# Performance work log

Hardware: AMD Instinct MI355X
Metric: run time of the kernel (lower is better)

Reference implementation:

```python
import jax, jax.numpy as jnp
import numpy as np

B, NF, EMB = 2048, 32, 64
FEAT_MAP_DIM = [128, 128, 128]  # split_half=True, activation=None


def setup_inputs() -> dict:
    key = jax.random.key(0)
    ks = jax.random.split(key, 7)
    inp = jax.random.normal(ks[0], (B, NF, EMB), dtype=jnp.float32)
    # conv1d_i: in_channels = H_{i-1} * NF, out_channels = FEAT_MAP_DIM[i]
    # H_0 = NF = 32; H_1 = H_2 = 128 // 2 = 64 (split_half)
    in_chs = [NF * NF, (FEAT_MAP_DIM[0] // 2) * NF, (FEAT_MAP_DIM[1] // 2) * NF]
    params = {}
    for i, (ic, oc) in enumerate(zip(in_chs, FEAT_MAP_DIM)):
        bound = 1.0 / np.sqrt(ic)  # torch Conv1d default init range
        params[f"W{i}"] = jax.random.uniform(ks[1 + 2 * i], (oc, ic), jnp.float32, -bound, bound)
        params[f"b{i}"] = jax.random.uniform(ks[2 + 2 * i], (oc,), jnp.float32, -bound, bound)
    return {"inp": inp, **params}


def reference(inp, W0, b0, W1, b1, W2, b2):
    # CIN: h_k[b,o,e] = sum_{j,z} W_k[o, j*NF+z] * h_{k-1}[b,j,e] * inp[b,z,e] + b_k[o]
    # The torch code materializes the outer product then applies a 1x1 conv;
    # the fused triple einsum below computes identical math.
    nf = inp.shape[1]
    Ws, bs = [W0, W1, W2], [b0, b1, b2]
    h = inp
    outs = []
    n_layers = len(Ws)
    for i, (W, b) in enumerate(zip(Ws, bs)):
        O, Hj = W.shape[0], h.shape[1]
        Wr = W.reshape(O, Hj, nf)  # channel index c = j*nf + z
        nxt = jnp.einsum('bjk,bzk,ojz->bok', h, inp, Wr) + b[None, :, None]
        if i != n_layers - 1:  # split_half
            h, o = nxt[:, : O // 2], nxt[:, O // 2 :]
        else:
            o = nxt
        outs.append(o)
    out = jnp.concatenate(outs, axis=1)  # (B, 64+64+128, EMB)
    return jnp.sum(out, axis=2)  # (B, 256)
```

## Files before the change

kernel.cpp:

```cpp
#include <hip/hip_runtime.h>


typedef _Float16 f16;
typedef _Float16 f16x4 __attribute__((ext_vector_type(4)));
typedef _Float16 f16x8 __attribute__((ext_vector_type(8)));
typedef float f32x4 __attribute__((ext_vector_type(4)));
typedef float f32x16 __attribute__((ext_vector_type(16)));

#define HSTR 72
#define PBS  5120

__device__ __forceinline__ f32x16 zero16() {
    f32x16 v;
#pragma unroll
    for (int i = 0; i < 16; ++i) v[i] = 0.0f;
    return v;
}

__global__ void __launch_bounds__(256)
prep_frag(const float* __restrict__ W0, const float* __restrict__ W1,
          const float* __restrict__ W2, f16* __restrict__ dst)
{
    int g = (blockIdx.x * 256 + threadIdx.x) * 8;
    const float* src; int base, KK, rbase;
    if (g < 65536)       { src = W0; base = 0;      KK = 64;  rbase = 0;  }
    else if (g < 131072) { src = W0; base = 65536;  KK = 64;  rbase = 64; }
    else if (g < 262144) { src = W1; base = 131072; KK = 128; rbase = 0;  }
    else if (g < 393216) { src = W1; base = 262144; KK = 128; rbase = 64; }
    else                 { src = W2; base = 393216; KK = 128; rbase = 0;  }
    int local = g - base;
    int frag  = local >> 9;
    int lane  = (local >> 3) & 63;
    int kk    = frag % KK;
    int mc    = frag / KK;
    int row   = rbase + mc * 32 + (lane & 31);
    int col   = kk * 16 + (lane >> 5) * 8;
    int IC    = KK * 16;
    const float* s = src + (size_t)row * IC + col;
    f16x8 o;
#pragma unroll
    for (int i = 0; i < 8; ++i) o[i] = (f16)s[i];
    *(f16x8*)(dst + g) = o;
}

__device__ __forceinline__ void p_chunk(const f16* __restrict__ hrows,
                                        const f16x8 (&pB)[4],
                                        f16* __restrict__ pdst, int t, int q)
{
    f32x16 acc = zero16();
#pragma unroll
    for (int s = 0; s < 4; ++s) {
        f16x8 a = *(const f16x8*)(hrows + t * HSTR + s * 16 + q * 8);
        acc = __builtin_amdgcn_mfma_f32_32x32x16_f16(a, pB[s], acc, 0, 0, 0);
    }
#pragma unroll
    for (int r = 0; r < 16; ++r) {
        int row = (r & 3) + 8 * (r >> 2) + 4 * q;
        pdst[row * 32 + t] = (f16)acc[r];
    }
}

template <int HJ>
__device__ __forceinline__ void h_gemm2(const f16* __restrict__ Hf,
                                        const f16* __restrict__ h0,
                                        const f16* __restrict__ h1,
                                        int lane8, int khOff,
                                        const f16x8 (&ip)[2][2],
                                        f32x16 (&acc)[2])
{
    acc[0] = zero16(); acc[1] = zero16();
    const f16* Wp = Hf + lane8;
    f16x8 wb[2][4];
    f16   sc[2][4];
#pragma unroll
    for (int ph = 0; ph < 2; ++ph)
#pragma unroll
        for (int jr = 0; jr < 2; ++jr) {
            int j = ph * 2 + jr;
            wb[ph][jr*2+0] = *(const f16x8*)(Wp + (j * 2 + 0) * 512);
            wb[ph][jr*2+1] = *(const f16x8*)(Wp + (j * 2 + 1) * 512);
            sc[ph][jr*2+0] = h0[j * HSTR + khOff];
            sc[ph][jr*2+1] = h1[j * HSTR + khOff];
        }
    for (int jj = 0; jj < HJ; jj += 4) {
#pragma unroll
        for (int ph = 0; ph < 2; ++ph) {
#pragma unroll
            for (int jr = 0; jr < 2; ++jr) {
                f16x8 w0 = wb[ph][jr*2+0], w1 = wb[ph][jr*2+1];
                f16 s0 = sc[ph][jr*2+0], s1 = sc[ph][jr*2+1];
                acc[0] = __builtin_amdgcn_mfma_f32_32x32x16_f16(w0, ip[0][0] * s0, acc[0], 0, 0, 0);
                acc[1] = __builtin_amdgcn_mfma_f32_32x32x16_f16(w0, ip[1][0] * s1, acc[1], 0, 0, 0);
                acc[0] = __builtin_amdgcn_mfma_f32_32x32x16_f16(w1, ip[0][1] * s0, acc[0], 0, 0, 0);
                acc[1] = __builtin_amdgcn_mfma_f32_32x32x16_f16(w1, ip[1][1] * s1, acc[1], 0, 0, 0);
            }
            int jn = jj + 4 + ph * 2;
            if (jn > HJ - 2) jn = HJ - 2;
#pragma unroll
            for (int jr = 0; jr < 2; ++jr) {
                int j = jn + jr;
                wb[ph][jr*2+0] = *(const f16x8*)(Wp + (j * 2 + 0) * 512);
                wb[ph][jr*2+1] = *(const f16x8*)(Wp + (j * 2 + 1) * 512);
                sc[ph][jr*2+0] = h0[j * HSTR + khOff];
                sc[ph][jr*2+1] = h1[j * HSTR + khOff];
            }
        }
    }
}

__device__ __forceinline__ void load_bias(const float* __restrict__ bl,
                                          float (&bve)[16], int g, int q)
{
#pragma unroll
    for (int r = 0; r < 16; ++r)
        bve[r] = bl[g * 32 + (r & 3) + 8 * (r >> 2) + 4 * q];
}

__device__ __forceinline__ void epi2(const f32x16 (&acc)[2], f16* __restrict__ hL,
                                     const float (&bve)[16], int g, int khOff,
                                     int t, int q)
{
#pragma unroll
    for (int r = 0; r < 16; ++r) {
        int row = g * 32 + (r & 3) + 8 * (r >> 2) + 4 * q;
        hL[row * HSTR + khOff]              = (f16)(acc[0][r] + bve[r]);
        hL[64 * HSTR + row * HSTR + khOff]  = (f16)(acc[1][r] + bve[r]);
    }
}

__global__ void __launch_bounds__(256, 4)
cin_h(const float* __restrict__ inp, const f16* __restrict__ Wf,
      f16* __restrict__ pW,
      const float* __restrict__ b0v, const float* __restrict__ b1v)
{
    __shared__ __attribute__((aligned(16))) f16 hL[2 * 64 * HSTR];

    const int tid   = threadIdx.x;
    const int w     = tid >> 6;
    const int lane  = tid & 63;
    const int t     = lane & 31;
    const int q     = lane >> 5;
    const int lane8 = lane * 8;
    const int kh    = w & 1;
    const int g     = w >> 1;
    const int khOff = kh * 32 + t;
    const int b0i   = blockIdx.x * 2;

#pragma unroll
    for (int it = 0; it < 4; ++it) {
        int idx = it * 1024 + tid * 4;
        int b = idx >> 11, rem = idx & 2047;
        int z = rem >> 6, k = rem & 63;
        f32x4 v = *(const f32x4*)(inp + (size_t)(b0i + b) * 2048 + rem);
        f16x4 h4;
        h4[0] = (f16)v[0]; h4[1] = (f16)v[1]; h4[2] = (f16)v[2]; h4[3] = (f16)v[3];
        *(f16x4*)(hL + b * 64 * HSTR + z * HSTR + k) = h4;
    }
    __syncthreads();

    f16x8 ip[2][2];
#pragma unroll
    for (int b = 0; b < 2; ++b)
#pragma unroll
        for (int kq = 0; kq < 2; ++kq) {
            f16x8 v;
            const f16* src = hL + b * 64 * HSTR;
#pragma unroll
            for (int i = 0; i < 8; ++i)
                v[i] = src[(kq * 16 + q * 8 + i) * HSTR + khOff];
            ip[b][kq] = v;
        }
    f16x8 pB[4];
#pragma unroll
    for (int s = 0; s < 4; ++s)
        pB[s] = *(const f16x8*)(hL + kh * 64 * HSTR + t * HSTR + s * 16 + q * 8);

    f16* pMy = pW + (size_t)(b0i + kh) * PBS;
    const f16* H0 = Wf;
    const f16* H1 = Wf + 131072;
    f32x16 acc[2];
    float bve[16];

    if (g == 0)
        p_chunk(hL + kh * 64 * HSTR, pB, pMy, t, q);
    h_gemm2<32>(H0 + g * 64 * 512, hL, hL + 64 * HSTR, lane8, khOff, ip, acc);
    load_bias(b0v, bve, g, q);
    __syncthreads();
    epi2(acc, hL, bve, g, khOff, t, q);
    __syncthreads();

    p_chunk(hL + kh * 64 * HSTR + g * 32 * HSTR, pB, pMy + 1024 + g * 1024, t, q);
    h_gemm2<64>(H1 + g * 128 * 512, hL, hL + 64 * HSTR, lane8, khOff, ip, acc);
    load_bias(b1v, bve, g, q);
    __syncthreads();
    epi2(acc, hL, bve, g, khOff, t, q);
    __syncthreads();

    p_chunk(hL + kh * 64 * HSTR + g * 32 * HSTR, pB, pMy + 3072 + g * 1024, t, q);
}

template <int S>
__device__ __forceinline__ void o_tile(const f16* __restrict__ Of,
                                       const f16* __restrict__ pBase,
                                       const float* __restrict__ biasp,
                                       float* __restrict__ out,
                                       float* __restrict__ rP,
                                       int bg, int colbase, int tid)
{
    const int w = tid >> 6, lane = tid & 63, t = lane & 31, q = lane >> 5;
    const int lane8 = lane * 8;
    const int mi = w & 1, ki = w >> 1;
    const f16* Ap = Of + (size_t)(mi * 2 * S + ki * S) * 512 + lane8;
    const f16* Bp = pBase + (size_t)(bg * 32 + t) * PBS + ki * S * 16 + q * 8;

    f32x16 acc = zero16();
    f16x8 af[4], bf[4];
#pragma unroll
    for (int i = 0; i < 4; ++i) {
        af[i] = *(const f16x8*)(Ap + i * 512);
        bf[i] = *(const f16x8*)(Bp + i * 16);
    }
#pragma unroll 4
    for (int s = 0; s < S; ++s) {
        int idx = s & 3;
        f16x8 a = af[idx], b = bf[idx];
        int sn = s + 4 < S ? s + 4 : S - 1;
        af[idx] = *(const f16x8*)(Ap + sn * 512);
        bf[idx] = *(const f16x8*)(Bp + sn * 16);
        acc = __builtin_amdgcn_mfma_f32_32x32x16_f16(a, b, acc, 0, 0, 0);
    }
#pragma unroll
    for (int r = 0; r < 16; ++r) {
        int m = mi * 32 + (r & 3) + 8 * (r >> 2) + 4 * q;
        rP[(ki * 32 + t) * 64 + m] = acc[r];
    }
    __syncthreads();
#pragma unroll
    for (int it = 0; it < 2; ++it) {
        int idx4 = (it * 256 + tid) * 4;
        int n = idx4 >> 6, o = idx4 & 63;
        f32x4 v0 = *(const f32x4*)(rP + n * 64 + o);
        f32x4 v1 = *(const f32x4*)(rP + (32 + n) * 64 + o);
        f32x4 bb = *(const f32x4*)(biasp + o);
        f32x4 ov;
        ov[0] = v0[0] + v1[0] + 64.0f * bb[0];
        ov[1] = v0[1] + v1[1] + 64.0f * bb[1];
        ov[2] = v0[2] + v1[2] + 64.0f * bb[2];
        ov[3] = v0[3] + v1[3] + 64.0f * bb[3];
        *(f32x4*)(out + (size_t)(bg * 32 + n) * 256 + colbase + o) = ov;
    }
}

__global__ void __launch_bounds__(256, 2)
cin_out(const f16* __restrict__ Wf, const f16* __restrict__ pW,
        const float* __restrict__ b0v, const float* __restrict__ b1v,
        const float* __restrict__ b2v, float* __restrict__ out)
{
    __shared__ __attribute__((aligned(16))) float rP[2 * 32 * 64];
    const int tid = threadIdx.x;
    const int r  = blockIdx.x & 3;
    const int bg = blockIdx.x >> 2;
    if (r == 0)
        o_tile<32>(Wf + 65536,  pW,        b0v + 64, out, rP, bg, 0,   tid);
    else if (r == 1)
        o_tile<64>(Wf + 262144, pW + 1024, b1v + 64, out, rP, bg, 64,  tid);
    else if (r == 2)
        o_tile<64>(Wf + 393216, pW + 3072, b2v,      out, rP, bg, 128, tid);
    else
        o_tile<64>(Wf + 524288, pW + 3072, b2v + 64, out, rP, bg, 192, tid);
}

extern "C" void kernel_launch(void* const* d_in, const int* in_sizes, int n_in,
                              void* d_out, int out_size, void* d_ws, size_t ws_size,
                              hipStream_t stream)
{
    const float* inp = (const float*)d_in[0];
    const float* W0  = (const float*)d_in[1];
    const float* b0  = (const float*)d_in[2];
    const float* W1  = (const float*)d_in[3];
    const float* b1  = (const float*)d_in[4];
    const float* W2  = (const float*)d_in[5];
    const float* b2  = (const float*)d_in[6];
    float* out = (float*)d_out;

    f16* Wf = (f16*)d_ws;
    f16* pW = Wf + 655360;

    prep_frag<<<320, 256, 0, stream>>>(W0, W1, W2, Wf);
    cin_h<<<1024, 256, 0, stream>>>(inp, Wf, pW, b0, b1);
    cin_out<<<256, 256, 0, stream>>>(Wf, pW, b0, b1, b2, out);
}
```

Before: 147.6 us.

## Process four batch samples per block in cin_h to reuse weight fragments

The hidden-layer kernel now handles four batch samples per block instead of two. Each wave covers both embedding halves for a pair of samples, so every loaded weight fragment feeds eight MFMAs instead of four. This halves the global weight traffic per sample and halves the grid size. In exchange it doubles LDS use, raises register pressure (launch bounds drop from 4 to 2 blocks per CU), and has every wave run the p_chunk projections.

```diff
diff --git a/kernel.cpp b/kernel.cpp
--- a/kernel.cpp
+++ b/kernel.cpp
@@ -61,49 +61,49 @@
 }
 
 template <int HJ>
-__device__ __forceinline__ void h_gemm2(const f16* __restrict__ Hf,
+__device__ __forceinline__ void h_gemm4(const f16* __restrict__ Hf,
                                         const f16* __restrict__ h0,
                                         const f16* __restrict__ h1,
-                                        int lane8, int khOff,
-                                        const f16x8 (&ip)[2][2],
-                                        f32x16 (&acc)[2])
-{
-    acc[0] = zero16(); acc[1] = zero16();
+                                        int lane8, int t,
+                                        const f16x8 (&ip)[2][2][2],
+                                        f32x16 (&acc)[2][2])
+{
+    acc[0][0] = zero16(); acc[0][1] = zero16();
+    acc[1][0] = zero16(); acc[1][1] = zero16();
     const f16* Wp = Hf + lane8;
-    f16x8 wb[2][4];
+    f16x8 wf[2][2];
     f16   sc[2][4];
 #pragma unroll
-    for (int ph = 0; ph < 2; ++ph)
-#pragma unroll
-        for (int jr = 0; jr < 2; ++jr) {
-            int j = ph * 2 + jr;
-            wb[ph][jr*2+0] = *(const f16x8*)(Wp + (j * 2 + 0) * 512);
-            wb[ph][jr*2+1] = *(const f16x8*)(Wp + (j * 2 + 1) * 512);
-            sc[ph][jr*2+0] = h0[j * HSTR + khOff];
-            sc[ph][jr*2+1] = h1[j * HSTR + khOff];
-        }
-    for (int jj = 0; jj < HJ; jj += 4) {
+    for (int ph = 0; ph < 2; ++ph) {
+        wf[ph][0] = *(const f16x8*)(Wp + (ph * 2 + 0) * 512);
+        wf[ph][1] = *(const f16x8*)(Wp + (ph * 2 + 1) * 512);
+        sc[ph][0] = h0[ph * HSTR + t];
+        sc[ph][1] = h0[ph * HSTR + 32 + t];
+        sc[ph][2] = h1[ph * HSTR + t];
+        sc[ph][3] = h1[ph * HSTR + 32 + t];
+    }
+    for (int jj = 0; jj < HJ; jj += 2) {
 #pragma unroll
         for (int ph = 0; ph < 2; ++ph) {
-#pragma unroll
-            for (int jr = 0; jr < 2; ++jr) {
-                f16x8 w0 = wb[ph][jr*2+0], w1 = wb[ph][jr*2+1];
-                f16 s0 = sc[ph][jr*2+0], s1 = sc[ph][jr*2+1];
-                acc[0] = __builtin_amdgcn_mfma_f32_32x32x16_f16(w0, ip[0][0] * s0, acc[0], 0, 0, 0);
-                acc[1] = __builtin_amdgcn_mfma_f32_32x32x16_f16(w0, ip[1][0] * s1, acc[1], 0, 0, 0);
-                acc[0] = __builtin_amdgcn_mfma_f32_32x32x16_f16(w1, ip[0][1] * s0, acc[0], 0, 0, 0);
-                acc[1] = __builtin_amdgcn_mfma_f32_32x32x16_f16(w1, ip[1][1] * s1, acc[1], 0, 0, 0);
-            }
-            int jn = jj + 4 + ph * 2;
-            if (jn > HJ - 2) jn = HJ - 2;
-#pragma unroll
-            for (int jr = 0; jr < 2; ++jr) {
-                int j = jn + jr;
-                wb[ph][jr*2+0] = *(const f16x8*)(Wp + (j * 2 + 0) * 512);
-                wb[ph][jr*2+1] = *(const f16x8*)(Wp + (j * 2 + 1) * 512);
-                sc[ph][jr*2+0] = h0[j * HSTR + khOff];
-                sc[ph][jr*2+1] = h1[j * HSTR + khOff];
-            }
+            f16x8 w0 = wf[ph][0], w1 = wf[ph][1];
+            f16 s00 = sc[ph][0], s01 = sc[ph][1];
+            f16 s10 = sc[ph][2], s11 = sc[ph][3];
+            int jn = jj + ph + 2;
+            if (jn > HJ - 1) jn = HJ - 1;
+            wf[ph][0] = *(const f16x8*)(Wp + (jn * 2 + 0) * 512);
+            wf[ph][1] = *(const f16x8*)(Wp + (jn * 2 + 1) * 512);
+            sc[ph][0] = h0[jn * HSTR + t];
+            sc[ph][1] = h0[jn * HSTR + 32 + t];
+            sc[ph][2] = h1[jn * HSTR + t];
+            sc[ph][3] = h1[jn * HSTR + 32 + t];
+            acc[0][0] = __builtin_amdgcn_mfma_f32_32x32x16_f16(w0, ip[0][0][0] * s00, acc[0][0], 0, 0, 0);
+            acc[0][0] = __builtin_amdgcn_mfma_f32_32x32x16_f16(w1, ip[0][1][0] * s00, acc[0][0], 0, 0, 0);
+            acc[0][1] = __builtin_amdgcn_mfma_f32_32x32x16_f16(w0, ip[0][0][1] * s01, acc[0][1], 0, 0, 0);
+            acc[0][1] = __builtin_amdgcn_mfma_f32_32x32x16_f16(w1, ip[0][1][1] * s01, acc[0][1], 0, 0, 0);
+            acc[1][0] = __builtin_amdgcn_mfma_f32_32x32x16_f16(w0, ip[1][0][0] * s10, acc[1][0], 0, 0, 0);
+            acc[1][0] = __builtin_amdgcn_mfma_f32_32x32x16_f16(w1, ip[1][1][0] * s10, acc[1][0], 0, 0, 0);
+            acc[1][1] = __builtin_amdgcn_mfma_f32_32x32x16_f16(w0, ip[1][0][1] * s11, acc[1][1], 0, 0, 0);
+            acc[1][1] = __builtin_amdgcn_mfma_f32_32x32x16_f16(w1, ip[1][1][1] * s11, acc[1][1], 0, 0, 0);
         }
     }
 }
@@ -116,24 +116,26 @@
         bve[r] = bl[g * 32 + (r & 3) + 8 * (r >> 2) + 4 * q];
 }
 
-__device__ __forceinline__ void epi2(const f32x16 (&acc)[2], f16* __restrict__ hL,
-                                     const float (&bve)[16], int g, int khOff,
-                                     int t, int q)
+__device__ __forceinline__ void epi4(const f32x16 (&acc)[2][2],
+                                     f16* __restrict__ h0d, f16* __restrict__ h1d,
+                                     const float (&bve)[16], int g, int t, int q)
 {
 #pragma unroll
     for (int r = 0; r < 16; ++r) {
         int row = g * 32 + (r & 3) + 8 * (r >> 2) + 4 * q;
-        hL[row * HSTR + khOff]              = (f16)(acc[0][r] + bve[r]);
-        hL[64 * HSTR + row * HSTR + khOff]  = (f16)(acc[1][r] + bve[r]);
-    }
-}
-
-__global__ void __launch_bounds__(256, 4)
+        h0d[row * HSTR + t]      = (f16)(acc[0][0][r] + bve[r]);
+        h0d[row * HSTR + 32 + t] = (f16)(acc[0][1][r] + bve[r]);
+        h1d[row * HSTR + t]      = (f16)(acc[1][0][r] + bve[r]);
+        h1d[row * HSTR + 32 + t] = (f16)(acc[1][1][r] + bve[r]);
+    }
+}
+
+__global__ void __launch_bounds__(256, 2)
 cin_h(const float* __restrict__ inp, const f16* __restrict__ Wf,
       f16* __restrict__ pW,
       const float* __restrict__ b0v, const float* __restrict__ b1v)
 {
-    __shared__ __attribute__((aligned(16))) f16 hL[2 * 64 * HSTR];
+    __shared__ __attribute__((aligned(16))) f16 hL[4 * 64 * HSTR];
 
     const int tid   = threadIdx.x;
     const int w     = tid >> 6;
@@ -141,13 +143,12 @@
     const int t     = lane & 31;
     const int q     = lane >> 5;
     const int lane8 = lane * 8;
-    const int kh    = w & 1;
+    const int bp    = w & 1;
     const int g     = w >> 1;
-    const int khOff = kh * 32 + t;
-    const int b0i   = blockIdx.x * 2;
-
-#pragma unroll
-    for (int it = 0; it < 4; ++it) {
+    const int b0i   = blockIdx.x * 4;
+
+#pragma unroll
+    for (int it = 0; it < 8; ++it) {
         int idx = it * 1024 + tid * 4;
         int b = idx >> 11, rem = idx & 2047;
         int z = rem >> 6, k = rem & 63;
@@ -158,45 +159,51 @@
     }
     __syncthreads();
 
-    f16x8 ip[2][2];
-#pragma unroll
-    for (int b = 0; b < 2; ++b)
-#pragma unroll
-        for (int kq = 0; kq < 2; ++kq) {
-            f16x8 v;
-            const f16* src = hL + b * 64 * HSTR;
-#pragma unroll
-            for (int i = 0; i < 8; ++i)
-                v[i] = src[(kq * 16 + q * 8 + i) * HSTR + khOff];
-            ip[b][kq] = v;
-        }
+    f16x8 ip[2][2][2];
+#pragma unroll
+    for (int b = 0; b < 2; ++b) {
+        const f16* src = hL + (bp * 2 + b) * 64 * HSTR;
+#pragma unroll
+        for (int kq = 0; kq < 2; ++kq)
+#pragma unroll
+            for (int nh = 0; nh < 2; ++nh) {
+                f16x8 v;
+#pragma unroll
+                for (int i = 0; i < 8; ++i)
+                    v[i] = src[(kq * 16 + q * 8 + i) * HSTR + nh * 32 + t];
+                ip[b][kq][nh] = v;
+            }
+    }
     f16x8 pB[4];
 #pragma unroll
     for (int s = 0; s < 4; ++s)
-        pB[s] = *(const f16x8*)(hL + kh * 64 * HSTR + t * HSTR + s * 16 + q * 8);
-
-    f16* pMy = pW + (size_t)(b0i + kh) * PBS;
+        pB[s] = *(const f16x8*)(hL + w * 64 * HSTR + t * HSTR + s * 16 + q * 8);
+
+    f16* pMy = pW + (size_t)(b0i + w) * PBS;
     const f16* H0 = Wf;
     const f16* H1 = Wf + 131072;
-    f32x16 acc[2];
+    f16* hA = hL + (bp * 2) * 64 * HSTR;
+    f16* hB = hL + (bp * 2 + 1) * 64 * HSTR;
+    f32x16 acc[2][2];
     float bve[16];
 
-    if (g == 0)
-        p_chunk(hL + kh * 64 * HSTR, pB, pMy, t, q);
-    h_gemm2<32>(H0 + g * 64 * 512, hL, hL + 64 * HSTR, lane8, khOff, ip, acc);
+    p_chunk(hL + w * 64 * HSTR, pB, pMy, t, q);
+    h_gemm4<32>(H0 + g * 64 * 512, hA, hB, lane8, t, ip, acc);
     load_bias(b0v, bve, g, q);
     __syncthreads();
-    epi2(acc, hL, bve, g, khOff, t, q);
-    __syncthreads();
-
-    p_chunk(hL + kh * 64 * HSTR + g * 32 * HSTR, pB, pMy + 1024 + g * 1024, t, q);
-    h_gemm2<64>(H1 + g * 128 * 512, hL, hL + 64 * HSTR, lane8, khOff, ip, acc);
+    epi4(acc, hA, hB, bve, g, t, q);
+    __syncthreads();
+
+    p_chunk(hL + w * 64 * HSTR,             pB, pMy + 1024, t, q);
+    p_chunk(hL + w * 64 * HSTR + 32 * HSTR, pB, pMy + 2048, t, q);
+    h_gemm4<64>(H1 + g * 128 * 512, hA, hB, lane8, t, ip, acc);
     load_bias(b1v, bve, g, q);
     __syncthreads();
-    epi2(acc, hL, bve, g, khOff, t, q);
-    __syncthreads();
-
-    p_chunk(hL + kh * 64 * HSTR + g * 32 * HSTR, pB, pMy + 3072 + g * 1024, t, q);
+    epi4(acc, hA, hB, bve, g, t, q);
+    __syncthreads();
+
+    p_chunk(hL + w * 64 * HSTR,             pB, pMy + 3072, t, q);
+    p_chunk(hL + w * 64 * HSTR + 32 * HSTR, pB, pMy + 4096, t, q);
 }
 
 template <int S>
@@ -287,6 +294,6 @@
     f16* pW = Wf + 655360;
 
     prep_frag<<<320, 256, 0, stream>>>(W0, W1, W2, Wf);
-    cin_h<<<1024, 256, 0, stream>>>(inp, Wf, pW, b0, b1);
+    cin_h<<<512, 256, 0, stream>>>(inp, Wf, pW, b0, b1);
     cin_out<<<256, 256, 0, stream>>>(Wf, pW, b0, b1, b2, out);
 }
```

New measurement: 138.3 us. 1.07x faster.
